# Performance work log

Measured on AMD Instinct MI355X. Metric: run time of the kernel, lower is better.

The kernel has to match this reference:

```python
import jax, jax.numpy as jnp
import numpy as np

B_SZ, L, DIM, H_DIM, D_STATE, K = 2, 2048, 768, 1536, 16, 4


def setup_inputs() -> dict:
    key = jax.random.key(0)
    ks = jax.random.split(key, 16)
    sc = 0.02
    inp = {
        "x": jax.random.normal(ks[0], (B_SZ, L, DIM), dtype=jnp.float32),
        "W1": jax.random.normal(ks[1], (DIM, H_DIM), dtype=jnp.float32) * sc,
        "b1": jnp.zeros((H_DIM,), dtype=jnp.float32),
        "W2": jax.random.normal(ks[2], (DIM, H_DIM), dtype=jnp.float32) * sc,
        "b2": jnp.zeros((H_DIM,), dtype=jnp.float32),
        "conv_w": jax.random.normal(ks[3], (H_DIM, 1, K), dtype=jnp.float32) * sc,  # depthwise, OIH
        "conv_b": jnp.zeros((H_DIM,), dtype=jnp.float32),
        "Wf": jax.random.normal(ks[4], (H_DIM, DIM), dtype=jnp.float32) * sc,
        "bf": jnp.zeros((DIM,), dtype=jnp.float32),
        "A": jnp.tile(jnp.arange(1, D_STATE + 1, dtype=jnp.float32), (H_DIM, 1)),  # [d, s]
        "WB": jax.random.normal(ks[5], (H_DIM, D_STATE), dtype=jnp.float32) * sc,
        "bB": jnp.zeros((D_STATE,), dtype=jnp.float32),
        "WC": jax.random.normal(ks[6], (H_DIM, D_STATE), dtype=jnp.float32) * sc,
        "bC": jnp.zeros((D_STATE,), dtype=jnp.float32),
        "WD": jax.random.normal(ks[7], (H_DIM, H_DIM), dtype=jnp.float32) * sc,
        "bD": jnp.zeros((H_DIM,), dtype=jnp.float32),
        "Dvec": jnp.ones((H_DIM,), dtype=jnp.float32),
    }
    return inp


def _forward(x, W1, b1, W2, b2, conv_w, conv_b, Wf, bf, A, WB, bB, WC, bC, WD, bD, Dvec):
    b, l, _ = x.shape
    k = conv_w.shape[-1]
    a = x @ W1 + b1                      # [b, l, d]
    g = jax.nn.silu(x @ W2 + b2)         # [b, l, d]  (silu(linear_2(x)))
    # depthwise causal conv1d: torch pads both sides by k-1 then slices [:l]
    xc = jnp.swapaxes(a, 1, 2)           # [b, d, l]
    ac = jax.lax.conv_general_dilated(
        xc, conv_w, window_strides=(1,), padding=[(k - 1, 0)],
        feature_group_count=xc.shape[1],
        dimension_numbers=("NCH", "OIH", "NCH"),
    ) + conv_b[None, :, None]
    a = jax.nn.silu(jnp.swapaxes(ac, 1, 2))          # [b, l, d]
    delta = jax.nn.softplus(Dvec + a @ WD + bD)       # [b, l, d]
    Bm = a @ WB + bB                                  # [b, l, s]
    # discretized dynamics
    A_ = jnp.exp(-A)[None, None] * delta[..., None]   # [b, l, d, s]
    X_ = Bm[:, :, None, :] * delta[..., None] * a[..., None]  # [b, l, d, s]
    # sequential selective scan: h_t = A_t * h_{t-1} + X_t
    A_t = jnp.moveaxis(A_, 1, 0)                      # [l, b, d, s]
    X_t = jnp.moveaxis(X_, 1, 0)
    def step(h, AX):
        At, Xt = AX
        h = At * h + Xt
        return h, h
    h0 = jnp.zeros(A_t.shape[1:], dtype=x.dtype)
    _, hs = jax.lax.scan(step, h0, (A_t, X_t))
    hid = jnp.moveaxis(hs, 0, 1)                      # [b, l, d, s]
    # NOTE: original computes einsum(hid, C) + D*a then overwrites it; the
    # returned output is linear_f(a * silu(linear_2(x))).
    output = (a * g) @ Wf + bf                        # [b, l, dim]
    return output, hid, a[..., 1:]


def reference(x, W1, b1, W2, b2, conv_w, conv_b, Wf, bf, A, WB, bB, WC, bC, WD, bD, Dvec):
    return _forward(x, W1, b1, W2, b2, conv_w, conv_b, Wf, bf, A, WB, bB, WC, bC, WD, bD, Dvec)
```

## Files before the change

### kernel.cpp

```cpp
#include <hip/hip_runtime.h>
#include <hip/hip_bf16.h>
#include <cstddef>

constexpr int B_SZ  = 2;
constexpr int LSEQ  = 2048;
constexpr int DIM   = 768;
constexpr int H_DIM = 1536;
constexpr int DST   = 16;
constexpr int KW    = 4;
constexpr int MROWS = B_SZ * LSEQ;
constexpr int HS    = H_DIM * DST;

constexpr int CCH  = 16;
constexpr int CLEN = LSEQ / CCH;

using short8 = __attribute__((ext_vector_type(8))) short;
using f32x4  = __attribute__((ext_vector_type(4))) float;

__device__ __forceinline__ short f2bf(float v) {
    union { float f; unsigned u; } x; x.f = v;
    unsigned r = (x.u + 0x7FFFu + ((x.u >> 16) & 1u)) >> 16;
    return (short)r;
}
__device__ __forceinline__ float bf2f(short s) {
    union { unsigned u; float f; } x; x.u = ((unsigned)(unsigned short)s) << 16;
    return x.f;
}

__global__ __launch_bounds__(256) void wsplit_k(
    const float* __restrict__ W, unsigned short* __restrict__ Wh,
    unsigned short* __restrict__ Wl, int K, int N)
{
    __shared__ float t[32][33];
    const int k0 = blockIdx.x * 32, n0 = blockIdx.y * 32;
    const int r = threadIdx.x >> 5, c = threadIdx.x & 31;
#pragma unroll
    for (int p = 0; p < 4; ++p)
        t[r + p * 8][c] = W[(size_t)(k0 + r + p * 8) * N + n0 + c];
    __syncthreads();
#pragma unroll
    for (int p = 0; p < 4; ++p) {
        int rr = r + p * 8;
        float v = t[c][rr];
        short hi = f2bf(v);
        short lo = f2bf(v - bf2f(hi));
        size_t o = (size_t)(n0 + rr) * K + k0 + c;
        Wh[o] = (unsigned short)hi;
        Wl[o] = (unsigned short)lo;
    }
}

__global__ __launch_bounds__(256) void xsplit_k(
    const float* __restrict__ X, unsigned short* __restrict__ Xh,
    unsigned short* __restrict__ Xl, size_t n8)
{
    size_t g = (size_t)blockIdx.x * 256 + threadIdx.x;
    if (g >= n8) return;
    const float* xp = X + g * 8;
    float v[8];
    *reinterpret_cast<float4*>(&v[0]) = *reinterpret_cast<const float4*>(xp);
    *reinterpret_cast<float4*>(&v[4]) = *reinterpret_cast<const float4*>(xp + 4);
    short h[8], l[8];
#pragma unroll
    for (int i = 0; i < 8; ++i) {
        h[i] = f2bf(v[i]);
        l[i] = f2bf(v[i] - bf2f(h[i]));
    }
    *reinterpret_cast<short8*>(Xh + g * 8) = *reinterpret_cast<short8*>(&h[0]);
    *reinterpret_cast<short8*>(Xl + g * 8) = *reinterpret_cast<short8*>(&l[0]);
}

template <int EPI>
__global__ __launch_bounds__(128) void gemm_bf(
    const unsigned short* __restrict__ Ahp, const unsigned short* __restrict__ Alp,
    const unsigned short* __restrict__ Bhp, const unsigned short* __restrict__ Blp,
    const float* __restrict__ bias, const float* __restrict__ extra,
    float* __restrict__ C, int M, int N, int K)
{
    constexpr int SK = 40;
    __shared__ short Ah[128 * SK], Al[128 * SK];
    __shared__ short Bh[64 * SK],  Bl[64 * SK];

    const int tid  = threadIdx.x;
    const int n0   = blockIdx.x * 64, m0 = blockIdx.y * 128;
    const int wave = tid >> 6, lane = tid & 63;
    const int lr   = lane & 15, kg = lane >> 4;

    f32x4 acc[4][4] = {};

    for (int k0 = 0; k0 < K; k0 += 32) {
        {
            const unsigned short* ah = Ahp + (size_t)(m0 + tid) * K + k0;
            const unsigned short* al = Alp + (size_t)(m0 + tid) * K + k0;
            int ab = tid * SK;
#pragma unroll
            for (int i = 0; i < 4; ++i) {
                *reinterpret_cast<short8*>(&Ah[ab + 8 * i]) =
                    *reinterpret_cast<const short8*>(ah + 8 * i);
                *reinterpret_cast<short8*>(&Al[ab + 8 * i]) =
                    *reinterpret_cast<const short8*>(al + 8 * i);
            }
        }
        {
            int brow = tid & 63;
            const unsigned short* bp =
                (tid < 64 ? Bhp : Blp) + (size_t)(n0 + brow) * K + k0;
            short* bd = (tid < 64 ? Bh : Bl) + brow * SK;
#pragma unroll
            for (int i = 0; i < 4; ++i)
                *reinterpret_cast<short8*>(&bd[8 * i]) =
                    *reinterpret_cast<const short8*>(bp + 8 * i);
        }
        __syncthreads();

        short8 fa_h[4], fa_l[4], fb_h[4], fb_l[4];
#pragma unroll
        for (int f = 0; f < 4; ++f) {
            int aoff = (wave * 64 + f * 16 + lr) * SK + kg * 8;
            int boff = (f * 16 + lr) * SK + kg * 8;
            fa_h[f] = *reinterpret_cast<const short8*>(&Ah[aoff]);
            fa_l[f] = *reinterpret_cast<const short8*>(&Al[aoff]);
            fb_h[f] = *reinterpret_cast<const short8*>(&Bh[boff]);
            fb_l[f] = *reinterpret_cast<const short8*>(&Bl[boff]);
        }
#pragma unroll
        for (int mf = 0; mf < 4; ++mf)
#pragma unroll
            for (int nf = 0; nf < 4; ++nf)
                acc[mf][nf] = __builtin_amdgcn_mfma_f32_16x16x32_bf16(
                    fa_h[mf], fb_h[nf], acc[mf][nf], 0, 0, 0);
#pragma unroll
        for (int mf = 0; mf < 4; ++mf)
#pragma unroll
            for (int nf = 0; nf < 4; ++nf)
                acc[mf][nf] = __builtin_amdgcn_mfma_f32_16x16x32_bf16(
                    fa_h[mf], fb_l[nf], acc[mf][nf], 0, 0, 0);
#pragma unroll
        for (int mf = 0; mf < 4; ++mf)
#pragma unroll
            for (int nf = 0; nf < 4; ++nf)
                acc[mf][nf] = __builtin_amdgcn_mfma_f32_16x16x32_bf16(
                    fa_l[mf], fb_h[nf], acc[mf][nf], 0, 0, 0);
        __syncthreads();
    }

    float bv[4], ev[4];
#pragma unroll
    for (int nf = 0; nf < 4; ++nf) {
        int col = n0 + nf * 16 + lr;
        bv[nf] = bias[col];
        ev[nf] = (EPI == 2) ? extra[col] : 0.f;
    }
#pragma unroll
    for (int mf = 0; mf < 4; ++mf)
#pragma unroll
        for (int nf = 0; nf < 4; ++nf) {
            int col = n0 + nf * 16 + lr;
#pragma unroll
            for (int r = 0; r < 4; ++r) {
                int mrow = m0 + wave * 64 + mf * 16 + kg * 4 + r;
                float v = acc[mf][nf][r] + bv[nf];
                if (EPI == 1) v = v / (1.f + expf(-v));
                if (EPI == 2) {
                    float t2 = ev[nf] + v;
                    v = fmaxf(t2, 0.f) + log1pf(expf(-fabsf(t2)));
                }
                C[(size_t)mrow * N + col] = v;
            }
        }
}

__global__ __launch_bounds__(256) void conv_k(
    const float* __restrict__ apre, const float* __restrict__ cw,
    const float* __restrict__ cb, const float* __restrict__ g,
    float* __restrict__ aout,
    unsigned short* __restrict__ ah, unsigned short* __restrict__ al,
    unsigned short* __restrict__ ph, unsigned short* __restrict__ pl,
    float* __restrict__ trim)
{
    int idx = blockIdx.x * 256 + threadIdx.x;
    int d  = idx % H_DIM;
    int bt = idx / H_DIM;
    int t  = bt % LSEQ;

    float4 w = *reinterpret_cast<const float4*>(cw + (size_t)d * KW);
    float acc = cb[d];
    if (t >= KW - 1) {
        const float* base = apre + (size_t)(bt - 3) * H_DIM + d;
        acc += base[0] * w.x;
        acc += base[H_DIM] * w.y;
        acc += base[2 * H_DIM] * w.z;
        acc += base[3 * H_DIM] * w.w;
    } else {
        const float* wp = reinterpret_cast<const float*>(&w);
#pragma unroll
        for (int j = 0; j < KW; ++j) {
            int tt = t + j - (KW - 1);
            if (tt >= 0) acc += apre[(size_t)(bt + j - 3) * H_DIM + d] * wp[j];
        }
    }
    float sv = acc / (1.f + expf(-acc));
    aout[idx] = sv;
    short h = f2bf(sv);
    ah[idx] = (unsigned short)h;
    al[idx] = (unsigned short)f2bf(sv - bf2f(h));
    float pv = sv * g[idx];
    short hp = f2bf(pv);
    ph[idx] = (unsigned short)hp;
    pl[idx] = (unsigned short)f2bf(pv - bf2f(hp));
    if (d >= 1)
        __builtin_nontemporal_store(sv, &trim[(size_t)bt * (H_DIM - 1) + d - 1]);
}

__global__ __launch_bounds__(256) void bm_k(
    const float* __restrict__ a, const float* __restrict__ WB,
    const float* __restrict__ bB, float* __restrict__ Bm)
{
    int g = blockIdx.x * 256 + threadIdx.x;
    int row = g >> 4, n = g & 15;
    const float* ar = a + (size_t)row * H_DIM;
    float a0 = 0.f, a1 = 0.f, a2 = 0.f, a3 = 0.f;
    for (int k = 0; k < H_DIM; k += 4) {
        a0 = fmaf(ar[k],     WB[(size_t)(k)*DST + n],     a0);
        a1 = fmaf(ar[k + 1], WB[(size_t)(k + 1)*DST + n], a1);
        a2 = fmaf(ar[k + 2], WB[(size_t)(k + 2)*DST + n], a2);
        a3 = fmaf(ar[k + 3], WB[(size_t)(k + 3)*DST + n], a3);
    }
    Bm[g] = bB[n] + ((a0 + a1) + (a2 + a3));
}

__global__ __launch_bounds__(256) void scan_a(
    const float* __restrict__ delta, const float* __restrict__ a,
    const float* __restrict__ Bm, const float* __restrict__ A,
    float* __restrict__ hend, float* __restrict__ Pout)
{
    int gtid = blockIdx.x * 256 + threadIdx.x;
    int ds = gtid % HS;
    int bc = gtid / HS;
    int c = bc % CCH, b = bc / CCH;
    int d = ds >> 4, s = ds & 15;

    float eA = expf(-A[ds]);
    float h = 0.f, P = 1.f;
    int bt0 = b * LSEQ + c * CLEN;
#pragma unroll 4
    for (int i = 0; i < CLEN; ++i) {
        int bt = bt0 + i;
        size_t ix = (size_t)bt * H_DIM + d;
        float dl = delta[ix];
        float av = a[ix];
        float bm = Bm[(size_t)bt * DST + s];
        float at = eA * dl;
        h = fmaf(at, h, bm * dl * av);
        P *= at;
    }
    size_t o = ((size_t)b * CCH + c) * HS + ds;
    hend[o] = h;
    Pout[o] = P;
}

__global__ __launch_bounds__(256) void scan_b(
    const float* __restrict__ hend, const float* __restrict__ P,
    float* __restrict__ Hinit)
{
    int gtid = blockIdx.x * 256 + threadIdx.x;
    int ds = gtid % HS;
    int b  = gtid / HS;
    float Hc = 0.f;
    for (int c = 0; c < CCH; ++c) {
        size_t o = ((size_t)b * CCH + c) * HS + ds;
        Hinit[o] = Hc;
        Hc = hend[o] + P[o] * Hc;
    }
}

__global__ __launch_bounds__(256) void scan_c(
    const float* __restrict__ delta, const float* __restrict__ a,
    const float* __restrict__ Bm, const float* __restrict__ A,
    const float* __restrict__ Hinit, float* __restrict__ hid)
{
    int gtid = blockIdx.x * 256 + threadIdx.x;
    int ds = gtid % HS;
    int bc = gtid / HS;
    int c = bc % CCH, b = bc / CCH;
    int d = ds >> 4, s = ds & 15;

    float eA = expf(-A[ds]);
    float h = Hinit[((size_t)b * CCH + c) * HS + ds];
    int bt0 = b * LSEQ + c * CLEN;
#pragma unroll 4
    for (int i = 0; i < CLEN; ++i) {
        int bt = bt0 + i;
        size_t ix = (size_t)bt * H_DIM + d;
        float dl = delta[ix];
        float av = a[ix];
        float bm = Bm[(size_t)bt * DST + s];
        float at = eA * dl;
        h = fmaf(at, h, bm * dl * av);
        __builtin_nontemporal_store(h, &hid[(size_t)bt * HS + ds]);
    }
}

extern "C" void kernel_launch(void* const* d_in, const int* in_sizes, int n_in,
                              void* d_out, int out_size, void* d_ws, size_t ws_size,
                              hipStream_t stream)
{
    const float* x      = (const float*)d_in[0];
    const float* W1     = (const float*)d_in[1];
    const float* b1     = (const float*)d_in[2];
    const float* W2     = (const float*)d_in[3];
    const float* b2     = (const float*)d_in[4];
    const float* conv_w = (const float*)d_in[5];
    const float* conv_b = (const float*)d_in[6];
    const float* Wf     = (const float*)d_in[7];
    const float* bf     = (const float*)d_in[8];
    const float* A      = (const float*)d_in[9];
    const float* WB     = (const float*)d_in[10];
    const float* bB     = (const float*)d_in[11];
    const float* WD     = (const float*)d_in[14];
    const float* bD     = (const float*)d_in[15];
    const float* Dvec   = (const float*)d_in[16];

    float* out = (float*)d_out;
    constexpr size_t OUT_HID  = (size_t)MROWS * DIM;
    constexpr size_t OUT_TRIM = OUT_HID + (size_t)MROWS * HS;
    float* out_y    = out;
    float* out_hid  = out + OUT_HID;
    float* out_trim = out + OUT_TRIM;

    constexpr size_t MH = (size_t)MROWS * H_DIM;
    constexpr size_t MD = (size_t)MROWS * DIM;
    float* a_pre = out_hid;
    float* g     = out_hid + MH;
    unsigned short* wsp = (unsigned short*)(out_hid + 2 * MH);
    constexpr size_t WSMALL = (size_t)H_DIM * DIM;
    constexpr size_t WBIG   = (size_t)H_DIM * H_DIM;
    unsigned short* W1h = wsp;            unsigned short* W1l = W1h + WSMALL;
    unsigned short* W2h = W1l + WSMALL;   unsigned short* W2l = W2h + WSMALL;
    unsigned short* WDh = W2l + WSMALL;   unsigned short* WDl = WDh + WBIG;
    unsigned short* Wfh = WDl + WBIG;     unsigned short* Wfl = Wfh + WSMALL;
    unsigned short* xh  = Wfl + WSMALL;   unsigned short* xl  = xh + MD;
    unsigned short* ah  = xl + MD;        unsigned short* al  = ah + MH;
    unsigned short* ph  = al + MH;        unsigned short* pl  = ph + MH;

    float* ws      = (float*)d_ws;
    float* a_ws    = ws;
    float* delta   = a_ws  + MH;
    float* Bm      = delta + MH;
    float* hend    = Bm    + (size_t)MROWS * DST;
    float* Pprod   = hend  + (size_t)B_SZ * HS * CCH;
    float* Hinit   = Pprod + (size_t)B_SZ * HS * CCH;

    dim3 blk(256);
    dim3 gblk(128);

    wsplit_k<<<dim3(DIM / 32, H_DIM / 32), blk, 0, stream>>>(W1, W1h, W1l, DIM, H_DIM);
    wsplit_k<<<dim3(DIM / 32, H_DIM / 32), blk, 0, stream>>>(W2, W2h, W2l, DIM, H_DIM);
    wsplit_k<<<dim3(H_DIM / 32, H_DIM / 32), blk, 0, stream>>>(WD, WDh, WDl, H_DIM, H_DIM);
    wsplit_k<<<dim3(H_DIM / 32, DIM / 32), blk, 0, stream>>>(Wf, Wfh, Wfl, H_DIM, DIM);
    xsplit_k<<<(unsigned)((MD / 8 + 255) / 256), blk, 0, stream>>>(x, xh, xl, MD / 8);

    gemm_bf<0><<<dim3(H_DIM / 64, MROWS / 128), gblk, 0, stream>>>(
        xh, xl, W1h, W1l, b1, nullptr, a_pre, MROWS, H_DIM, DIM);
    gemm_bf<1><<<dim3(H_DIM / 64, MROWS / 128), gblk, 0, stream>>>(
        xh, xl, W2h, W2l, b2, nullptr, g, MROWS, H_DIM, DIM);
    conv_k<<<(MROWS * H_DIM) / 256, blk, 0, stream>>>(
        a_pre, conv_w, conv_b, g, a_ws, ah, al, ph, pl, out_trim);
    gemm_bf<2><<<dim3(H_DIM / 64, MROWS / 128), gblk, 0, stream>>>(
        ah, al, WDh, WDl, bD, Dvec, delta, MROWS, H_DIM, H_DIM);
    bm_k<<<(MROWS * DST) / 256, blk, 0, stream>>>(a_ws, WB, bB, Bm);
    gemm_bf<0><<<dim3(DIM / 64, MROWS / 128), gblk, 0, stream>>>(
        ph, pl, Wfh, Wfl, bf, nullptr, out_y, MROWS, DIM, H_DIM);
    scan_a<<<(B_SZ * CCH * HS) / 256, blk, 0, stream>>>(delta, a_ws, Bm, A, hend, Pprod);
    scan_b<<<(B_SZ * HS) / 256, blk, 0, stream>>>(hend, Pprod, Hinit);
    scan_c<<<(B_SZ * CCH * HS) / 256, blk, 0, stream>>>(delta, a_ws, Bm, A, Hinit, out_hid);
}
```

Before: 1.022 ms.

## Replace LDS-staged GEMM with single-wave register-direct MFMA GEMM

The split-bf16 GEMM no longer stages A and B tiles through shared memory with barriers. Each 64-thread block (one wave) now computes a 64x64 tile and loads MFMA fragments straight from global memory into registers. This removes the LDS traffic and the __syncthreads stalls and doubles the number of blocks. In exchange, data reuse across waves is lost, each fragment load is a strided 16-byte global read, and the kernel relies on L1/L2 caching to serve the reused tiles.

```diff
diff --git a/kernel.cpp b/kernel.cpp
--- a/kernel.cpp
+++ b/kernel.cpp
@@ -71,57 +71,33 @@
 }
 
 template <int EPI>
-__global__ __launch_bounds__(128) void gemm_bf(
+__global__ __launch_bounds__(64) void gemm_reg(
     const unsigned short* __restrict__ Ahp, const unsigned short* __restrict__ Alp,
     const unsigned short* __restrict__ Bhp, const unsigned short* __restrict__ Blp,
     const float* __restrict__ bias, const float* __restrict__ extra,
     float* __restrict__ C, int M, int N, int K)
 {
-    constexpr int SK = 40;
-    __shared__ short Ah[128 * SK], Al[128 * SK];
-    __shared__ short Bh[64 * SK],  Bl[64 * SK];
-
-    const int tid  = threadIdx.x;
-    const int n0   = blockIdx.x * 64, m0 = blockIdx.y * 128;
-    const int wave = tid >> 6, lane = tid & 63;
-    const int lr   = lane & 15, kg = lane >> 4;
+    const int lane = threadIdx.x;
+    const int n0 = blockIdx.x * 64, m0 = blockIdx.y * 64;
+    const int lr = lane & 15, kg = lane >> 4;
+
+    size_t aoff[4], boff[4];
+#pragma unroll
+    for (int f = 0; f < 4; ++f) {
+        aoff[f] = (size_t)(m0 + f * 16 + lr) * K + kg * 8;
+        boff[f] = (size_t)(n0 + f * 16 + lr) * K + kg * 8;
+    }
 
     f32x4 acc[4][4] = {};
 
     for (int k0 = 0; k0 < K; k0 += 32) {
-        {
-            const unsigned short* ah = Ahp + (size_t)(m0 + tid) * K + k0;
-            const unsigned short* al = Alp + (size_t)(m0 + tid) * K + k0;
-            int ab = tid * SK;
-#pragma unroll
-            for (int i = 0; i < 4; ++i) {
-                *reinterpret_cast<short8*>(&Ah[ab + 8 * i]) =
-                    *reinterpret_cast<const short8*>(ah + 8 * i);
-                *reinterpret_cast<short8*>(&Al[ab + 8 * i]) =
-                    *reinterpret_cast<const short8*>(al + 8 * i);
-            }
-        }
-        {
-            int brow = tid & 63;
-            const unsigned short* bp =
-                (tid < 64 ? Bhp : Blp) + (size_t)(n0 + brow) * K + k0;
-            short* bd = (tid < 64 ? Bh : Bl) + brow * SK;
-#pragma unroll
-            for (int i = 0; i < 4; ++i)
-                *reinterpret_cast<short8*>(&bd[8 * i]) =
-                    *reinterpret_cast<const short8*>(bp + 8 * i);
-        }
-        __syncthreads();
-
         short8 fa_h[4], fa_l[4], fb_h[4], fb_l[4];
 #pragma unroll
         for (int f = 0; f < 4; ++f) {
-            int aoff = (wave * 64 + f * 16 + lr) * SK + kg * 8;
-            int boff = (f * 16 + lr) * SK + kg * 8;
-            fa_h[f] = *reinterpret_cast<const short8*>(&Ah[aoff]);
-            fa_l[f] = *reinterpret_cast<const short8*>(&Al[aoff]);
-            fb_h[f] = *reinterpret_cast<const short8*>(&Bh[boff]);
-            fb_l[f] = *reinterpret_cast<const short8*>(&Bl[boff]);
+            fa_h[f] = *reinterpret_cast<const short8*>(Ahp + aoff[f] + k0);
+            fa_l[f] = *reinterpret_cast<const short8*>(Alp + aoff[f] + k0);
+            fb_h[f] = *reinterpret_cast<const short8*>(Bhp + boff[f] + k0);
+            fb_l[f] = *reinterpret_cast<const short8*>(Blp + boff[f] + k0);
         }
 #pragma unroll
         for (int mf = 0; mf < 4; ++mf)
@@ -141,7 +117,6 @@
             for (int nf = 0; nf < 4; ++nf)
                 acc[mf][nf] = __builtin_amdgcn_mfma_f32_16x16x32_bf16(
                     fa_l[mf], fb_h[nf], acc[mf][nf], 0, 0, 0);
-        __syncthreads();
     }
 
     float bv[4], ev[4];
@@ -158,7 +133,7 @@
             int col = n0 + nf * 16 + lr;
 #pragma unroll
             for (int r = 0; r < 4; ++r) {
-                int mrow = m0 + wave * 64 + mf * 16 + kg * 4 + r;
+                int mrow = m0 + mf * 16 + kg * 4 + r;
                 float v = acc[mf][nf][r] + bv[nf];
                 if (EPI == 1) v = v / (1.f + expf(-v));
                 if (EPI == 2) {
@@ -352,7 +327,7 @@
     float* Hinit   = Pprod + (size_t)B_SZ * HS * CCH;
 
     dim3 blk(256);
-    dim3 gblk(128);
+    dim3 wblk(64);
 
     wsplit_k<<<dim3(DIM / 32, H_DIM / 32), blk, 0, stream>>>(W1, W1h, W1l, DIM, H_DIM);
     wsplit_k<<<dim3(DIM / 32, H_DIM / 32), blk, 0, stream>>>(W2, W2h, W2l, DIM, H_DIM);
@@ -360,16 +335,16 @@
     wsplit_k<<<dim3(H_DIM / 32, DIM / 32), blk, 0, stream>>>(Wf, Wfh, Wfl, H_DIM, DIM);
     xsplit_k<<<(unsigned)((MD / 8 + 255) / 256), blk, 0, stream>>>(x, xh, xl, MD / 8);
 
-    gemm_bf<0><<<dim3(H_DIM / 64, MROWS / 128), gblk, 0, stream>>>(
+    gemm_reg<0><<<dim3(H_DIM / 64, MROWS / 64), wblk, 0, stream>>>(
         xh, xl, W1h, W1l, b1, nullptr, a_pre, MROWS, H_DIM, DIM);
-    gemm_bf<1><<<dim3(H_DIM / 64, MROWS / 128), gblk, 0, stream>>>(
+    gemm_reg<1><<<dim3(H_DIM / 64, MROWS / 64), wblk, 0, stream>>>(
         xh, xl, W2h, W2l, b2, nullptr, g, MROWS, H_DIM, DIM);
     conv_k<<<(MROWS * H_DIM) / 256, blk, 0, stream>>>(
         a_pre, conv_w, conv_b, g, a_ws, ah, al, ph, pl, out_trim);
-    gemm_bf<2><<<dim3(H_DIM / 64, MROWS / 128), gblk, 0, stream>>>(
+    gemm_reg<2><<<dim3(H_DIM / 64, MROWS / 64), wblk, 0, stream>>>(
         ah, al, WDh, WDl, bD, Dvec, delta, MROWS, H_DIM, H_DIM);
     bm_k<<<(MROWS * DST) / 256, blk, 0, stream>>>(a_ws, WB, bB, Bm);
-    gemm_bf<0><<<dim3(DIM / 64, MROWS / 128), gblk, 0, stream>>>(
+    gemm_reg<0><<<dim3(DIM / 64, MROWS / 64), wblk, 0, stream>>>(
         ph, pl, Wfh, Wfl, bf, nullptr, out_y, MROWS, DIM, H_DIM);
     scan_a<<<(B_SZ * CCH * HS) / 256, blk, 0, stream>>>(delta, a_ws, Bm, A, hend, Pprod);
     scan_b<<<(B_SZ * HS) / 256, blk, 0, stream>>>(hend, Pprod, Hinit);
```

Result: faster. 998.5 us (-2.3%).
